# Kernel optimization log

Measured on AMD Instinct MI355X. Metric: run time of the kernel, lower is better.

## Reference

```python
import jax, jax.numpy as jnp
import numpy as np

EMBED_DIM = 1024
NUM_HEADS = 16
HEAD_DIM = EMBED_DIM // NUM_HEADS


def setup_inputs() -> dict:
    key = jax.random.key(0)
    k1, k2, k3, k4 = jax.random.split(key, 4)
    x = jax.random.normal(k1, (2, 2048, EMBED_DIM), dtype=jnp.float32)
    # nn.Linear weights: stored as [out, in]; we keep that convention.
    s = 1.0 / np.sqrt(EMBED_DIM)
    w_qkv = jax.random.uniform(k2, (3 * EMBED_DIM, EMBED_DIM), jnp.float32, -s, s)
    w_proj = jax.random.uniform(k3, (EMBED_DIM, EMBED_DIM), jnp.float32, -s, s)
    b_proj = jax.random.uniform(k4, (EMBED_DIM,), jnp.float32, -s, s)
    return {"x": x, "w_qkv": w_qkv, "w_proj": w_proj, "b_proj": b_proj}


def reference(x, w_qkv, w_proj, b_proj):
    B, N, C = x.shape
    H, D = NUM_HEADS, HEAD_DIM
    scale = D ** -0.5
    # qkv: [B, N, 3C] -> [3, B, H, N, D]
    qkv = jnp.einsum('bnc,oc->bno', x, w_qkv)
    qkv = qkv.reshape(B, N, 3, H, D).transpose(2, 0, 3, 1, 4)
    q, k, v = qkv[0] * scale, qkv[1], qkv[2]
    attn = jax.nn.softmax(jnp.einsum('bhnd,bhmd->bhnm', q, k), axis=-1)
    out = jnp.einsum('bhnm,bhmd->bhnd', attn, v)
    out = out.transpose(0, 2, 1, 3).reshape(B, N, C)
    return jnp.einsum('bnc,oc->bno', out, w_proj) + b_proj
```

## Files before the change

kernel.cpp:

```cpp
#include <hip/hip_runtime.h>


constexpr int B_ = 2, N_ = 2048, C_ = 1024, H_ = 16, D_ = 64;
constexpr int M_ = B_ * N_;
constexpr int O3 = 3 * C_;
constexpr int KVB = 64;
constexpr int NTILES = N_ / KVB;

typedef short bf16x8 __attribute__((ext_vector_type(8)));
typedef _Float16 half8 __attribute__((ext_vector_type(8)));
typedef _Float16 half4v __attribute__((ext_vector_type(4)));
typedef float f32x4  __attribute__((ext_vector_type(4)));

__device__ __forceinline__ unsigned short f2bf(float f) {
    unsigned int u = __float_as_uint(f);
    unsigned int r = (u + 0x7FFFu + ((u >> 16) & 1u)) >> 16;
    return (unsigned short)r;
}

__device__ __forceinline__ void async16(const void* g, void* l) {
    __builtin_amdgcn_global_load_lds(
        (const __attribute__((address_space(1))) unsigned int*)g,
        (__attribute__((address_space(3))) unsigned int*)l, 16, 0, 0);
}

constexpr size_t XN  = (size_t)M_ * C_;
constexpr size_t WQN = (size_t)O3 * C_;
constexpr size_t WPN = (size_t)C_ * C_;

__global__ __launch_bounds__(256)
void convert_f16(const float* __restrict__ x, const float* __restrict__ wq,
                 const float* __restrict__ wp, _Float16* __restrict__ dst)
{
    size_t i = ((size_t)blockIdx.x * 256 + threadIdx.x) * 8;
    const float* src;
    size_t off;
    if (i < XN)            { src = x;  off = i; }
    else if (i < XN + WQN) { src = wq; off = i - XN; }
    else                   { src = wp; off = i - XN - WQN; }
    float4 a = *(const float4*)(src + off);
    float4 b = *(const float4*)(src + off + 4);
    half8 h;
    h[0] = (_Float16)a.x; h[1] = (_Float16)a.y; h[2] = (_Float16)a.z; h[3] = (_Float16)a.w;
    h[4] = (_Float16)b.x; h[5] = (_Float16)b.y; h[6] = (_Float16)b.z; h[7] = (_Float16)b.w;
    *(half8*)(dst + i) = h;
}

template<int MODE>
__global__ __launch_bounds__(256)
void gemm128(const _Float16* __restrict__ Ag, const _Float16* __restrict__ Bg,
             unsigned short* __restrict__ Qd, unsigned short* __restrict__ Kd,
             unsigned short* __restrict__ Vt,
             const float* __restrict__ bias, float* __restrict__ Out)
{
    __shared__ __align__(16) unsigned char Ab[2][16384];
    __shared__ __align__(16) unsigned char Bb[2][16384];

    const int t    = threadIdx.x;
    const int lane = t & 63;
    const int w    = t >> 6;
    const int g    = lane >> 4;
    const int c    = lane & 15;
    const int wm   = w >> 1, wn = w & 1;
    const int bm   = blockIdx.y * 128;
    const int bn   = blockIdx.x * 128;
    constexpr int K = C_;

    f32x4 acc[4][4];
    f32x4 zero = {0.f, 0.f, 0.f, 0.f};
    #pragma unroll
    for (int mi = 0; mi < 4; ++mi)
        #pragma unroll
        for (int ni = 0; ni < 4; ++ni) acc[mi][ni] = zero;

    auto stage = [&](int buf, int k0) {
        #pragma unroll
        for (int i = 0; i < 4; ++i) {
            int id  = t + 256 * i;
            int row = id >> 3;
            int p   = id & 7;
            int gs  = p ^ (row & 7);
            async16(Ag + (size_t)(bm + row) * K + k0 + 8 * gs, &Ab[buf][id * 16]);
            async16(Bg + (size_t)(bn + row) * K + k0 + 8 * gs, &Bb[buf][id * 16]);
        }
    };

    stage(0, 0);
    __syncthreads();
    int cur = 0;

    for (int k0 = 0; k0 < K; k0 += 64) {
        if (k0 + 64 < K) stage(cur ^ 1, k0 + 64);

        const unsigned char* Abase = Ab[cur];
        const unsigned char* Bbase = Bb[cur];
        #pragma unroll
        for (int s = 0; s < 2; ++s) {
            half8 af[4], bf[4];
            #pragma unroll
            for (int mi = 0; mi < 4; ++mi) {
                int row = wm * 64 + mi * 16 + c;
                af[mi] = *(const half8*)(Abase + (row * 8 + ((s * 4 + g) ^ (row & 7))) * 16);
            }
            #pragma unroll
            for (int ni = 0; ni < 4; ++ni) {
                int row = wn * 64 + ni * 16 + c;
                bf[ni] = *(const half8*)(Bbase + (row * 8 + ((s * 4 + g) ^ (row & 7))) * 16);
            }
            #pragma unroll
            for (int mi = 0; mi < 4; ++mi)
                #pragma unroll
                for (int ni = 0; ni < 4; ++ni)
                    acc[mi][ni] = __builtin_amdgcn_mfma_f32_16x16x32_f16(af[mi], bf[ni], acc[mi][ni], 0, 0, 0);
        }

        __syncthreads();
        cur ^= 1;
    }

    if constexpr (MODE == 0) {
        constexpr float QSCALE = 0.125f * 1.4426950408889634f;
        const int o0 = bn + wn * 64;
        const int which = o0 >> 10;
        const int h  = (o0 & 1023) >> 6;
        const int m0 = bm + wm * 64;
        const int b  = m0 >> 11;
        const int n0 = m0 & 2047;
        const size_t bh = (size_t)b * H_ + h;
        if (which == 0) {
            unsigned short* base = Qd + (bh * N_) * D_;
            #pragma unroll
            for (int mi = 0; mi < 4; ++mi)
                #pragma unroll
                for (int ni = 0; ni < 4; ++ni)
                    #pragma unroll
                    for (int r = 0; r < 4; ++r)
                        base[(size_t)(n0 + mi * 16 + 4 * g + r) * D_ + ni * 16 + c] =
                            f2bf(acc[mi][ni][r] * QSCALE);
        } else if (which == 1) {
            unsigned short* base = Kd + (bh * N_) * D_;
            #pragma unroll
            for (int mi = 0; mi < 4; ++mi)
                #pragma unroll
                for (int ni = 0; ni < 4; ++ni)
                    #pragma unroll
                    for (int r = 0; r < 4; ++r)
                        base[(size_t)(n0 + mi * 16 + 4 * g + r) * D_ + ni * 16 + c] =
                            f2bf(acc[mi][ni][r]);
        } else {
            unsigned short* base = Vt + (bh * D_) * (size_t)N_;
            #pragma unroll
            for (int mi = 0; mi < 4; ++mi)
                #pragma unroll
                for (int ni = 0; ni < 4; ++ni) {
                    ushort4 v;
                    v.x = f2bf(acc[mi][ni][0]);
                    v.y = f2bf(acc[mi][ni][1]);
                    v.z = f2bf(acc[mi][ni][2]);
                    v.w = f2bf(acc[mi][ni][3]);
                    *(ushort4*)&base[(size_t)(ni * 16 + c) * N_ + n0 + mi * 16 + 4 * g] = v;
                }
        }
    } else {
        const int m0 = bm + wm * 64;
        const int o0 = bn + wn * 64;
        #pragma unroll
        for (int ni = 0; ni < 4; ++ni) {
            float bb = bias[o0 + ni * 16 + c];
            #pragma unroll
            for (int mi = 0; mi < 4; ++mi)
                #pragma unroll
                for (int r = 0; r < 4; ++r)
                    Out[(size_t)(m0 + mi * 16 + 4 * g + r) * C_ + o0 + ni * 16 + c] =
                        acc[mi][ni][r] + bb;
        }
    }
}

__global__ __launch_bounds__(512)
void attn_mfma(const unsigned short* __restrict__ Qd, const unsigned short* __restrict__ Kd,
               const unsigned short* __restrict__ Vt, _Float16* __restrict__ AO)
{
    __shared__ __align__(16) unsigned char KsB[2][64 * 128];
    __shared__ __align__(16) unsigned char VtB[2][64 * 128];
    __shared__ __align__(16) unsigned char Pb[8][16 * 128];

    const int t    = threadIdx.x;
    const int lane = t & 63;
    const int w    = t >> 6;
    const int g    = lane >> 4;
    const int c    = lane & 15;
    const int cx   = c & 7;

    int flat = blockIdx.x;
    int work = (flat & 7) * 64 + (flat >> 3);
    const int bh = work >> 4;
    const int qt = work & 15;
    const int b  = bh >> 4, h = bh & 15;
    const int q0 = qt * 128;

    const unsigned short* Kp = Kd + (size_t)bh * N_ * D_;
    const unsigned short* Vp = Vt + (size_t)bh * D_ * N_;

    const unsigned short* qp = Qd + ((size_t)bh * N_ + q0 + w * 16 + c) * D_;
    bf16x8 qf0 = *(const bf16x8*)(qp + 8 * g);
    bf16x8 qf1 = *(const bf16x8*)(qp + 32 + 8 * g);

    const int rk = t >> 3, pk = t & 7;
    const unsigned char* kSrc = (const unsigned char*)Kp + rk * 128 + ((pk ^ (rk & 7)) << 4);
    const unsigned char* vSrc = (const unsigned char*)Vp + (size_t)rk * N_ * 2 + ((pk ^ (rk & 7)) << 4);
    unsigned char* kDstA = KsB[0] + t * 16;
    unsigned char* kDstB = KsB[1] + t * 16;
    unsigned char* vDstA = VtB[0] + t * 16;
    unsigned char* vDstB = VtB[1] + t * 16;

    bf16x8 aone;
    {
        short onev = (c == 0) ? (short)0x3F80 : (short)0;
        #pragma unroll
        for (int e = 0; e < 8; ++e) aone[e] = onev;
    }

    float m_run = -1e30f;
    f32x4 oc[4];
    f32x4 lsum;
    f32x4 zero = {0.f, 0.f, 0.f, 0.f};
    #pragma unroll
    for (int dc = 0; dc < 4; ++dc) oc[dc] = zero;
    lsum = zero;

    async16(kSrc, kDstA);
    async16(vSrc, vDstA);
    __syncthreads();

    unsigned char* pw  = Pb[w] + c * 128;
    const unsigned char* prd = Pb[w] + c * 128;

    auto tile_body = [&](const unsigned char* kbase, const unsigned char* vb,
                         unsigned char* kDstN, unsigned char* vDstN, int ktNext) {
        if (ktNext < NTILES) {
            async16(kSrc + (size_t)ktNext * KVB * 128, kDstN);
            async16(vSrc + (size_t)ktNext * 128, vDstN);
        }

        f32x4 st[4];
        #pragma unroll
        for (int tt = 0; tt < 4; ++tt) st[tt] = zero;
        __builtin_amdgcn_s_setprio(1);
        #pragma unroll
        for (int s = 0; s < 2; ++s) {
            bf16x8 qf = s ? qf1 : qf0;
            #pragma unroll
            for (int tt = 0; tt < 4; ++tt) {
                bf16x8 a = *(const bf16x8*)(kbase + (tt * 16 + c) * 128 + (((4 * s + g) ^ cx) << 4));
                st[tt] = __builtin_amdgcn_mfma_f32_16x16x32_bf16(a, qf, st[tt], 0, 0, 0);
            }
        }
        __builtin_amdgcn_s_setprio(0);

        float t0 = fmaxf(fmaxf(st[0][0], st[0][1]), st[0][2]);
        float t1 = fmaxf(fmaxf(st[0][3], st[1][0]), st[1][1]);
        float t2 = fmaxf(fmaxf(st[1][2], st[1][3]), st[2][0]);
        float t3 = fmaxf(fmaxf(st[2][1], st[2][2]), st[2][3]);
        float t4 = fmaxf(fmaxf(st[3][0], st[3][1]), st[3][2]);
        float mx = fmaxf(fmaxf(fmaxf(t0, t1), fmaxf(t2, t3)), fmaxf(t4, st[3][3]));
        mx = fmaxf(mx, __shfl_xor(mx, 16));
        mx = fmaxf(mx, __shfl_xor(mx, 32));

        const bool defer = __all(mx <= m_run + 8.f);
        if (!defer) {
            const float nm = fmaxf(m_run, mx);
            const float corr = exp2f(m_run - nm);
            m_run = nm;
            #pragma unroll
            for (int dc = 0; dc < 4; ++dc) oc[dc] *= corr;
            lsum[0] *= corr;
        }
        const float nm = m_run;
        #pragma unroll
        for (int tt = 0; tt < 4; ++tt)
            #pragma unroll
            for (int r = 0; r < 4; ++r)
                st[tt][r] = exp2f(st[tt][r] - nm);

        #pragma unroll
        for (int tt = 0; tt < 4; ++tt) {
            unsigned int lo = __byte_perm(__float_as_uint(st[tt][0]), __float_as_uint(st[tt][1]), 0x7632);
            unsigned int hi = __byte_perm(__float_as_uint(st[tt][2]), __float_as_uint(st[tt][3]), 0x7632);
            int gran = 2 * tt + (g >> 1);
            unsigned int* dst = (unsigned int*)(pw + ((gran ^ cx) << 4) + 8 * (g & 1));
            dst[0] = lo;
            dst[1] = hi;
        }

        bf16x8 pb0 = *(const bf16x8*)(prd + ((g ^ cx) << 4));
        bf16x8 pb1 = *(const bf16x8*)(prd + (((4 + g) ^ cx) << 4));
        __builtin_amdgcn_s_setprio(1);
        #pragma unroll
        for (int dc = 0; dc < 4; ++dc) {
            const unsigned char* vrow = vb + (dc * 16 + c) * 128;
            bf16x8 a0 = *(const bf16x8*)(vrow + ((g ^ cx) << 4));
            bf16x8 a1 = *(const bf16x8*)(vrow + (((4 + g) ^ cx) << 4));
            oc[dc] = __builtin_amdgcn_mfma_f32_16x16x32_bf16(a0, pb0, oc[dc], 0, 0, 0);
            oc[dc] = __builtin_amdgcn_mfma_f32_16x16x32_bf16(a1, pb1, oc[dc], 0, 0, 0);
        }
        lsum = __builtin_amdgcn_mfma_f32_16x16x32_bf16(aone, pb0, lsum, 0, 0, 0);
        lsum = __builtin_amdgcn_mfma_f32_16x16x32_bf16(aone, pb1, lsum, 0, 0, 0);
        __builtin_amdgcn_s_setprio(0);

        __syncthreads();
    };

    #pragma unroll 1
    for (int kt = 0; kt < NTILES; kt += 2) {
        tile_body(KsB[0], VtB[0], kDstB, vDstB, kt + 1);
        tile_body(KsB[1], VtB[1], kDstA, vDstA, kt + 2);
    }

    float l = __shfl(lsum[0], c);
    float inv = 1.0f / l;
    int q = q0 + w * 16 + c;
    _Float16* aop = AO + ((size_t)b * N_ + q) * C_ + h * D_;
    #pragma unroll
    for (int dc = 0; dc < 4; ++dc) {
        half4v o;
        o[0] = (_Float16)(oc[dc][0] * inv);
        o[1] = (_Float16)(oc[dc][1] * inv);
        o[2] = (_Float16)(oc[dc][2] * inv);
        o[3] = (_Float16)(oc[dc][3] * inv);
        *(half4v*)(aop + dc * 16 + 4 * g) = o;
    }
}

extern "C" void kernel_launch(void* const* d_in, const int* in_sizes, int n_in,
                              void* d_out, int out_size, void* d_ws, size_t ws_size,
                              hipStream_t stream) {
    const float* x      = (const float*)d_in[0];
    const float* w_qkv  = (const float*)d_in[1];
    const float* w_proj = (const float*)d_in[2];
    const float* b_proj = (const float*)d_in[3];
    float* out = (float*)d_out;

    const size_t hd = (size_t)B_ * H_ * N_ * D_;
    unsigned short* Qd = (unsigned short*)d_ws;
    unsigned short* Kd = Qd + hd;
    unsigned short* Vt = Kd + hd;
    _Float16* AO  = (_Float16*)(Vt + hd);
    _Float16* x16 = AO + hd;
    _Float16* wq16 = x16 + XN;
    _Float16* wp16 = wq16 + WQN;

    convert_f16<<<4096, 256, 0, stream>>>(x, w_qkv, w_proj, x16);
    gemm128<0><<<dim3(O3 / 128, M_ / 128), 256, 0, stream>>>(
        x16, wq16, Qd, Kd, Vt, nullptr, nullptr);
    attn_mfma<<<dim3(512), 512, 0, stream>>>(Qd, Kd, Vt, AO);
    gemm128<1><<<dim3(C_ / 128, M_ / 128), 256, 0, stream>>>(
        AO, wp16, nullptr, nullptr, nullptr, b_proj, out);
}
```

Measured before the change: 134.6 us.

## Process two 16-row query sub-tiles per wave to reuse K/V LDS fragments

Each wave in the attention kernel now handles 32 query rows (two 16-row sub-tiles) instead of 16, so each block covers 256 queries and the grid halves to 256 blocks. Every K and V fragment read from LDS feeds two MFMAs, halving LDS traffic and global K/V loads per query. The cost is roughly doubled accumulator and score registers per lane, larger LDS buffers for P, and only 256 blocks on a 256-CU device, which may reduce occupancy and latency hiding.

```diff
diff --git a/kernel.cpp b/kernel.cpp
--- a/kernel.cpp
+++ b/kernel.cpp
@@ -177,13 +177,13 @@
     }
 }
 
-__global__ __launch_bounds__(512)
+__global__ __launch_bounds__(512, 2)
 void attn_mfma(const unsigned short* __restrict__ Qd, const unsigned short* __restrict__ Kd,
                const unsigned short* __restrict__ Vt, _Float16* __restrict__ AO)
 {
-    __shared__ __align__(16) unsigned char KsB[2][64 * 128];
-    __shared__ __align__(16) unsigned char VtB[2][64 * 128];
-    __shared__ __align__(16) unsigned char Pb[8][16 * 128];
+    __shared__ __align__(16) unsigned char KsB[2][8192];
+    __shared__ __align__(16) unsigned char VtB[2][8192];
+    __shared__ __align__(16) unsigned char Pb[8][4096];
 
     const int t    = threadIdx.x;
     const int lane = t & 63;
@@ -193,18 +193,22 @@
     const int cx   = c & 7;
 
     int flat = blockIdx.x;
-    int work = (flat & 7) * 64 + (flat >> 3);
-    const int bh = work >> 4;
-    const int qt = work & 15;
+    int work = (flat & 7) * 32 + (flat >> 3);
+    const int bh = work >> 3;
+    const int qt = work & 7;
     const int b  = bh >> 4, h = bh & 15;
-    const int q0 = qt * 128;
+    const int q0 = qt * 256;
 
     const unsigned short* Kp = Kd + (size_t)bh * N_ * D_;
     const unsigned short* Vp = Vt + (size_t)bh * D_ * N_;
 
-    const unsigned short* qp = Qd + ((size_t)bh * N_ + q0 + w * 16 + c) * D_;
-    bf16x8 qf0 = *(const bf16x8*)(qp + 8 * g);
-    bf16x8 qf1 = *(const bf16x8*)(qp + 32 + 8 * g);
+    const unsigned short* qp = Qd + ((size_t)bh * N_ + q0 + w * 32 + c) * D_;
+    bf16x8 qf[2][2];
+    #pragma unroll
+    for (int qs = 0; qs < 2; ++qs)
+        #pragma unroll
+        for (int s = 0; s < 2; ++s)
+            qf[qs][s] = *(const bf16x8*)(qp + qs * 16 * D_ + s * 32 + 8 * g);
 
     const int rk = t >> 3, pk = t & 7;
     const unsigned char* kSrc = (const unsigned char*)Kp + rk * 128 + ((pk ^ (rk & 7)) << 4);
@@ -221,20 +225,20 @@
         for (int e = 0; e < 8; ++e) aone[e] = onev;
     }
 
-    float m_run = -1e30f;
-    f32x4 oc[4];
-    f32x4 lsum;
+    float m_run[2] = {-1e30f, -1e30f};
+    f32x4 oc[2][4];
+    f32x4 lsum[2];
     f32x4 zero = {0.f, 0.f, 0.f, 0.f};
     #pragma unroll
-    for (int dc = 0; dc < 4; ++dc) oc[dc] = zero;
-    lsum = zero;
+    for (int qs = 0; qs < 2; ++qs) {
+        lsum[qs] = zero;
+        #pragma unroll
+        for (int dc = 0; dc < 4; ++dc) oc[qs][dc] = zero;
+    }
 
     async16(kSrc, kDstA);
     async16(vSrc, vDstA);
     __syncthreads();
-
-    unsigned char* pw  = Pb[w] + c * 128;
-    const unsigned char* prd = Pb[w] + c * 128;
 
     auto tile_body = [&](const unsigned char* kbase, const unsigned char* vb,
                          unsigned char* kDstN, unsigned char* vDstN, int ktNext) {
@@ -243,69 +247,86 @@
             async16(vSrc + (size_t)ktNext * 128, vDstN);
         }
 
-        f32x4 st[4];
-        #pragma unroll
-        for (int tt = 0; tt < 4; ++tt) st[tt] = zero;
+        f32x4 st[2][4];
+        #pragma unroll
+        for (int qs = 0; qs < 2; ++qs)
+            #pragma unroll
+            for (int tt = 0; tt < 4; ++tt) st[qs][tt] = zero;
         __builtin_amdgcn_s_setprio(1);
         #pragma unroll
         for (int s = 0; s < 2; ++s) {
-            bf16x8 qf = s ? qf1 : qf0;
             #pragma unroll
             for (int tt = 0; tt < 4; ++tt) {
                 bf16x8 a = *(const bf16x8*)(kbase + (tt * 16 + c) * 128 + (((4 * s + g) ^ cx) << 4));
-                st[tt] = __builtin_amdgcn_mfma_f32_16x16x32_bf16(a, qf, st[tt], 0, 0, 0);
+                st[0][tt] = __builtin_amdgcn_mfma_f32_16x16x32_bf16(a, qf[0][s], st[0][tt], 0, 0, 0);
+                st[1][tt] = __builtin_amdgcn_mfma_f32_16x16x32_bf16(a, qf[1][s], st[1][tt], 0, 0, 0);
             }
         }
         __builtin_amdgcn_s_setprio(0);
 
-        float t0 = fmaxf(fmaxf(st[0][0], st[0][1]), st[0][2]);
-        float t1 = fmaxf(fmaxf(st[0][3], st[1][0]), st[1][1]);
-        float t2 = fmaxf(fmaxf(st[1][2], st[1][3]), st[2][0]);
-        float t3 = fmaxf(fmaxf(st[2][1], st[2][2]), st[2][3]);
-        float t4 = fmaxf(fmaxf(st[3][0], st[3][1]), st[3][2]);
-        float mx = fmaxf(fmaxf(fmaxf(t0, t1), fmaxf(t2, t3)), fmaxf(t4, st[3][3]));
-        mx = fmaxf(mx, __shfl_xor(mx, 16));
-        mx = fmaxf(mx, __shfl_xor(mx, 32));
-
-        const bool defer = __all(mx <= m_run + 8.f);
+        float mx[2];
+        #pragma unroll
+        for (int qs = 0; qs < 2; ++qs) {
+            float t0 = fmaxf(fmaxf(st[qs][0][0], st[qs][0][1]), st[qs][0][2]);
+            float t1 = fmaxf(fmaxf(st[qs][0][3], st[qs][1][0]), st[qs][1][1]);
+            float t2 = fmaxf(fmaxf(st[qs][1][2], st[qs][1][3]), st[qs][2][0]);
+            float t3 = fmaxf(fmaxf(st[qs][2][1], st[qs][2][2]), st[qs][2][3]);
+            float t4 = fmaxf(fmaxf(st[qs][3][0], st[qs][3][1]), st[qs][3][2]);
+            float m  = fmaxf(fmaxf(fmaxf(t0, t1), fmaxf(t2, t3)), fmaxf(t4, st[qs][3][3]));
+            m = fmaxf(m, __shfl_xor(m, 16));
+            m = fmaxf(m, __shfl_xor(m, 32));
+            mx[qs] = m;
+        }
+
+        const bool defer = __all(fmaxf(mx[0] - m_run[0], mx[1] - m_run[1]) <= 8.f);
         if (!defer) {
-            const float nm = fmaxf(m_run, mx);
-            const float corr = exp2f(m_run - nm);
-            m_run = nm;
-            #pragma unroll
-            for (int dc = 0; dc < 4; ++dc) oc[dc] *= corr;
-            lsum[0] *= corr;
-        }
-        const float nm = m_run;
-        #pragma unroll
-        for (int tt = 0; tt < 4; ++tt)
-            #pragma unroll
-            for (int r = 0; r < 4; ++r)
-                st[tt][r] = exp2f(st[tt][r] - nm);
-
-        #pragma unroll
-        for (int tt = 0; tt < 4; ++tt) {
-            unsigned int lo = __byte_perm(__float_as_uint(st[tt][0]), __float_as_uint(st[tt][1]), 0x7632);
-            unsigned int hi = __byte_perm(__float_as_uint(st[tt][2]), __float_as_uint(st[tt][3]), 0x7632);
-            int gran = 2 * tt + (g >> 1);
-            unsigned int* dst = (unsigned int*)(pw + ((gran ^ cx) << 4) + 8 * (g & 1));
-            dst[0] = lo;
-            dst[1] = hi;
-        }
-
-        bf16x8 pb0 = *(const bf16x8*)(prd + ((g ^ cx) << 4));
-        bf16x8 pb1 = *(const bf16x8*)(prd + (((4 + g) ^ cx) << 4));
+            #pragma unroll
+            for (int qs = 0; qs < 2; ++qs) {
+                const float nm = fmaxf(m_run[qs], mx[qs]);
+                const float corr = exp2f(m_run[qs] - nm);
+                m_run[qs] = nm;
+                #pragma unroll
+                for (int dc = 0; dc < 4; ++dc) oc[qs][dc] *= corr;
+                lsum[qs][0] *= corr;
+            }
+        }
+        #pragma unroll
+        for (int qs = 0; qs < 2; ++qs)
+            #pragma unroll
+            for (int tt = 0; tt < 4; ++tt)
+                #pragma unroll
+                for (int r = 0; r < 4; ++r)
+                    st[qs][tt][r] = exp2f(st[qs][tt][r] - m_run[qs]);
+
+        #pragma unroll
+        for (int qs = 0; qs < 2; ++qs) {
+            unsigned char* pwq = Pb[w] + qs * 2048 + c * 128;
+            #pragma unroll
+            for (int tt = 0; tt < 4; ++tt) {
+                unsigned int lo = __byte_perm(__float_as_uint(st[qs][tt][0]), __float_as_uint(st[qs][tt][1]), 0x7632);
+                unsigned int hi = __byte_perm(__float_as_uint(st[qs][tt][2]), __float_as_uint(st[qs][tt][3]), 0x7632);
+                int gran = 2 * tt + (g >> 1);
+                unsigned int* dst = (unsigned int*)(pwq + ((gran ^ cx) << 4) + 8 * (g & 1));
+                dst[0] = lo;
+                dst[1] = hi;
+            }
+        }
+
+        const unsigned char* prd = Pb[w] + c * 128;
         __builtin_amdgcn_s_setprio(1);
         #pragma unroll
-        for (int dc = 0; dc < 4; ++dc) {
-            const unsigned char* vrow = vb + (dc * 16 + c) * 128;
-            bf16x8 a0 = *(const bf16x8*)(vrow + ((g ^ cx) << 4));
-            bf16x8 a1 = *(const bf16x8*)(vrow + (((4 + g) ^ cx) << 4));
-            oc[dc] = __builtin_amdgcn_mfma_f32_16x16x32_bf16(a0, pb0, oc[dc], 0, 0, 0);
-            oc[dc] = __builtin_amdgcn_mfma_f32_16x16x32_bf16(a1, pb1, oc[dc], 0, 0, 0);
-        }
-        lsum = __builtin_amdgcn_mfma_f32_16x16x32_bf16(aone, pb0, lsum, 0, 0, 0);
-        lsum = __builtin_amdgcn_mfma_f32_16x16x32_bf16(aone, pb1, lsum, 0, 0, 0);
+        for (int s = 0; s < 2; ++s) {
+            bf16x8 pb0 = *(const bf16x8*)(prd + (((s * 4 + g) ^ cx) << 4));
+            bf16x8 pb1 = *(const bf16x8*)(prd + 2048 + (((s * 4 + g) ^ cx) << 4));
+            #pragma unroll
+            for (int dc = 0; dc < 4; ++dc) {
+                bf16x8 a = *(const bf16x8*)(vb + (dc * 16 + c) * 128 + (((s * 4 + g) ^ cx) << 4));
+                oc[0][dc] = __builtin_amdgcn_mfma_f32_16x16x32_bf16(a, pb0, oc[0][dc], 0, 0, 0);
+                oc[1][dc] = __builtin_amdgcn_mfma_f32_16x16x32_bf16(a, pb1, oc[1][dc], 0, 0, 0);
+            }
+            lsum[0] = __builtin_amdgcn_mfma_f32_16x16x32_bf16(aone, pb0, lsum[0], 0, 0, 0);
+            lsum[1] = __builtin_amdgcn_mfma_f32_16x16x32_bf16(aone, pb1, lsum[1], 0, 0, 0);
+        }
         __builtin_amdgcn_s_setprio(0);
 
         __syncthreads();
@@ -317,18 +338,21 @@
         tile_body(KsB[1], VtB[1], kDstA, vDstA, kt + 2);
     }
 
-    float l = __shfl(lsum[0], c);
-    float inv = 1.0f / l;
-    int q = q0 + w * 16 + c;
-    _Float16* aop = AO + ((size_t)b * N_ + q) * C_ + h * D_;
     #pragma unroll
-    for (int dc = 0; dc < 4; ++dc) {
-        half4v o;
-        o[0] = (_Float16)(oc[dc][0] * inv);
-        o[1] = (_Float16)(oc[dc][1] * inv);
-        o[2] = (_Float16)(oc[dc][2] * inv);
-        o[3] = (_Float16)(oc[dc][3] * inv);
-        *(half4v*)(aop + dc * 16 + 4 * g) = o;
+    for (int qs = 0; qs < 2; ++qs) {
+        float l = __shfl(lsum[qs][0], c);
+        float inv = 1.0f / l;
+        int q = q0 + w * 32 + qs * 16 + c;
+        _Float16* aop = AO + ((size_t)b * N_ + q) * C_ + h * D_;
+        #pragma unroll
+        for (int dc = 0; dc < 4; ++dc) {
+            half4v o;
+            o[0] = (_Float16)(oc[qs][dc][0] * inv);
+            o[1] = (_Float16)(oc[qs][dc][1] * inv);
+            o[2] = (_Float16)(oc[qs][dc][2] * inv);
+            o[3] = (_Float16)(oc[qs][dc][3] * inv);
+            *(half4v*)(aop + dc * 16 + 4 * g) = o;
+        }
     }
 }
 
@@ -353,7 +377,7 @@
     convert_f16<<<4096, 256, 0, stream>>>(x, w_qkv, w_proj, x16);
     gemm128<0><<<dim3(O3 / 128, M_ / 128), 256, 0, stream>>>(
         x16, wq16, Qd, Kd, Vt, nullptr, nullptr);
-    attn_mfma<<<dim3(512), 512, 0, stream>>>(Qd, Kd, Vt, AO);
+    attn_mfma<<<dim3(256), 512, 0, stream>>>(Qd, Kd, Vt, AO);
     gemm128<1><<<dim3(C_ / 128, M_ / 128), 256, 0, stream>>>(
         AO, wp16, nullptr, nullptr, nullptr, b_proj, out);
 }
```

Result: slower. 140.2 us (+4.1%).

## Switch attention to 32x32x16 MFMA with register-resident P via permlane32 swap

Applied to the files above, without the earlier changes.

The attention kernel now uses 32x32x16 bf16 MFMA instead of 16x16x32, with 4 waves of 256 threads each handling 32 query rows. The softmax probabilities stay in registers and are rearranged with v_permlane32_swap into the B operand layout, so the per-wave LDS staging buffer and its round trip go away. The row sum is computed with VALU adds plus a shuffle, replacing the extra ones-vector MFMAs. The goal is fewer LDS accesses and MFMA instructions per tile. The cost is more accumulator registers per wave and twice the async loads per thread.

```diff
diff --git a/kernel.cpp b/kernel.cpp
--- a/kernel.cpp
+++ b/kernel.cpp
@@ -11,6 +11,7 @@
 typedef _Float16 half8 __attribute__((ext_vector_type(8)));
 typedef _Float16 half4v __attribute__((ext_vector_type(4)));
 typedef float f32x4  __attribute__((ext_vector_type(4)));
+typedef float f32x16 __attribute__((ext_vector_type(16)));
 
 __device__ __forceinline__ unsigned short f2bf(float f) {
     unsigned int u = __float_as_uint(f);
@@ -177,94 +178,84 @@
     }
 }
 
-__global__ __launch_bounds__(512)
+__global__ __launch_bounds__(256, 2)
 void attn_mfma(const unsigned short* __restrict__ Qd, const unsigned short* __restrict__ Kd,
                const unsigned short* __restrict__ Vt, _Float16* __restrict__ AO)
 {
-    __shared__ __align__(16) unsigned char KsB[2][64 * 128];
-    __shared__ __align__(16) unsigned char VtB[2][64 * 128];
-    __shared__ __align__(16) unsigned char Pb[8][16 * 128];
+    __shared__ __align__(16) unsigned char KsB[2][8192];
+    __shared__ __align__(16) unsigned char VtB[2][8192];
 
     const int t    = threadIdx.x;
     const int lane = t & 63;
     const int w    = t >> 6;
-    const int g    = lane >> 4;
-    const int c    = lane & 15;
-    const int cx   = c & 7;
+    const int h    = lane >> 5;
+    const int q31  = lane & 31;
+    const int qsw  = q31 & 7;
 
     int flat = blockIdx.x;
     int work = (flat & 7) * 64 + (flat >> 3);
     const int bh = work >> 4;
     const int qt = work & 15;
-    const int b  = bh >> 4, h = bh & 15;
+    const int b  = bh >> 4, hh = bh & 15;
     const int q0 = qt * 128;
 
     const unsigned short* Kp = Kd + (size_t)bh * N_ * D_;
     const unsigned short* Vp = Vt + (size_t)bh * D_ * N_;
 
-    const unsigned short* qp = Qd + ((size_t)bh * N_ + q0 + w * 16 + c) * D_;
-    bf16x8 qf0 = *(const bf16x8*)(qp + 8 * g);
-    bf16x8 qf1 = *(const bf16x8*)(qp + 32 + 8 * g);
+    const unsigned short* qp = Qd + ((size_t)bh * N_ + q0 + w * 32 + q31) * D_;
+    bf16x8 qf[4];
+    #pragma unroll
+    for (int s = 0; s < 4; ++s)
+        qf[s] = *(const bf16x8*)(qp + 16 * s + 8 * h);
 
     const int rk = t >> 3, pk = t & 7;
     const unsigned char* kSrc = (const unsigned char*)Kp + rk * 128 + ((pk ^ (rk & 7)) << 4);
-    const unsigned char* vSrc = (const unsigned char*)Vp + (size_t)rk * N_ * 2 + ((pk ^ (rk & 7)) << 4);
+    const unsigned char* vSrc = (const unsigned char*)Vp + (size_t)rk * (N_ * 2) + ((pk ^ (rk & 7)) << 4);
     unsigned char* kDstA = KsB[0] + t * 16;
     unsigned char* kDstB = KsB[1] + t * 16;
     unsigned char* vDstA = VtB[0] + t * 16;
     unsigned char* vDstB = VtB[1] + t * 16;
 
-    bf16x8 aone;
-    {
-        short onev = (c == 0) ? (short)0x3F80 : (short)0;
-        #pragma unroll
-        for (int e = 0; e < 8; ++e) aone[e] = onev;
-    }
-
-    float m_run = -1e30f;
-    f32x4 oc[4];
-    f32x4 lsum;
-    f32x4 zero = {0.f, 0.f, 0.f, 0.f};
-    #pragma unroll
-    for (int dc = 0; dc < 4; ++dc) oc[dc] = zero;
-    lsum = zero;
-
-    async16(kSrc, kDstA);
-    async16(vSrc, vDstA);
+    float m_run = -1e30f, l_run = 0.f;
+    f32x16 oc0 = 0.f, oc1 = 0.f;
+
+    auto stage = [&](unsigned char* kD, unsigned char* vD, int kt) {
+        async16(kSrc + (size_t)kt * 8192, kD);
+        async16(kSrc + (size_t)kt * 8192 + 4096, kD + 4096);
+        async16(vSrc + (size_t)kt * 128, vD);
+        async16(vSrc + 32 * (size_t)(N_ * 2) + (size_t)kt * 128, vD + 4096);
+    };
+
+    stage(kDstA, vDstA, 0);
     __syncthreads();
 
-    unsigned char* pw  = Pb[w] + c * 128;
-    const unsigned char* prd = Pb[w] + c * 128;
-
-    auto tile_body = [&](const unsigned char* kbase, const unsigned char* vb,
+    auto tile_body = [&](const unsigned char* kbase, const unsigned char* vbase,
                          unsigned char* kDstN, unsigned char* vDstN, int ktNext) {
-        if (ktNext < NTILES) {
-            async16(kSrc + (size_t)ktNext * KVB * 128, kDstN);
-            async16(vSrc + (size_t)ktNext * 128, vDstN);
-        }
-
-        f32x4 st[4];
-        #pragma unroll
-        for (int tt = 0; tt < 4; ++tt) st[tt] = zero;
+        if (ktNext < NTILES) stage(kDstN, vDstN, ktNext);
+
+        f32x16 st0 = 0.f, st1 = 0.f;
+        const unsigned char* krow0 = kbase + q31 * 128;
+        const unsigned char* krow1 = kbase + (32 + q31) * 128;
         __builtin_amdgcn_s_setprio(1);
         #pragma unroll
-        for (int s = 0; s < 2; ++s) {
-            bf16x8 qf = s ? qf1 : qf0;
-            #pragma unroll
-            for (int tt = 0; tt < 4; ++tt) {
-                bf16x8 a = *(const bf16x8*)(kbase + (tt * 16 + c) * 128 + (((4 * s + g) ^ cx) << 4));
-                st[tt] = __builtin_amdgcn_mfma_f32_16x16x32_bf16(a, qf, st[tt], 0, 0, 0);
-            }
+        for (int s = 0; s < 4; ++s) {
+            int go = ((2 * s + h) ^ qsw) << 4;
+            bf16x8 a0 = *(const bf16x8*)(krow0 + go);
+            bf16x8 a1 = *(const bf16x8*)(krow1 + go);
+            st0 = __builtin_amdgcn_mfma_f32_32x32x16_bf16(a0, qf[s], st0, 0, 0, 0);
+            st1 = __builtin_amdgcn_mfma_f32_32x32x16_bf16(a1, qf[s], st1, 0, 0, 0);
         }
         __builtin_amdgcn_s_setprio(0);
 
-        float t0 = fmaxf(fmaxf(st[0][0], st[0][1]), st[0][2]);
-        float t1 = fmaxf(fmaxf(st[0][3], st[1][0]), st[1][1]);
-        float t2 = fmaxf(fmaxf(st[1][2], st[1][3]), st[2][0]);
-        float t3 = fmaxf(fmaxf(st[2][1], st[2][2]), st[2][3]);
-        float t4 = fmaxf(fmaxf(st[3][0], st[3][1]), st[3][2]);
-        float mx = fmaxf(fmaxf(fmaxf(t0, t1), fmaxf(t2, t3)), fmaxf(t4, st[3][3]));
-        mx = fmaxf(mx, __shfl_xor(mx, 16));
+        f32x16 mm;
+        #pragma unroll
+        for (int r = 0; r < 16; ++r) mm[r] = fmaxf(st0[r], st1[r]);
+        float a0 = fmaxf(fmaxf(mm[0], mm[1]), mm[2]);
+        float a1 = fmaxf(fmaxf(mm[3], mm[4]), mm[5]);
+        float a2 = fmaxf(fmaxf(mm[6], mm[7]), mm[8]);
+        float a3 = fmaxf(fmaxf(mm[9], mm[10]), mm[11]);
+        float a4 = fmaxf(fmaxf(mm[12], mm[13]), mm[14]);
+        float mx = fmaxf(fmaxf(fmaxf(a0, a1), fmaxf(a2, a3)), fmaxf(a4, mm[15]));
         mx = fmaxf(mx, __shfl_xor(mx, 32));
 
         const bool defer = __all(mx <= m_run + 8.f);
@@ -272,40 +263,65 @@
             const float nm = fmaxf(m_run, mx);
             const float corr = exp2f(m_run - nm);
             m_run = nm;
-            #pragma unroll
-            for (int dc = 0; dc < 4; ++dc) oc[dc] *= corr;
-            lsum[0] *= corr;
-        }
-        const float nm = m_run;
-        #pragma unroll
-        for (int tt = 0; tt < 4; ++tt)
-            #pragma unroll
-            for (int r = 0; r < 4; ++r)
-                st[tt][r] = exp2f(st[tt][r] - nm);
-
-        #pragma unroll
-        for (int tt = 0; tt < 4; ++tt) {
-            unsigned int lo = __byte_perm(__float_as_uint(st[tt][0]), __float_as_uint(st[tt][1]), 0x7632);
-            unsigned int hi = __byte_perm(__float_as_uint(st[tt][2]), __float_as_uint(st[tt][3]), 0x7632);
-            int gran = 2 * tt + (g >> 1);
-            unsigned int* dst = (unsigned int*)(pw + ((gran ^ cx) << 4) + 8 * (g & 1));
-            dst[0] = lo;
-            dst[1] = hi;
-        }
-
-        bf16x8 pb0 = *(const bf16x8*)(prd + ((g ^ cx) << 4));
-        bf16x8 pb1 = *(const bf16x8*)(prd + (((4 + g) ^ cx) << 4));
+            oc0 *= corr;
+            oc1 *= corr;
+            l_run *= corr;
+        }
+        #pragma unroll
+        for (int r = 0; r < 16; ++r) {
+            st0[r] = exp2f(st0[r] - m_run);
+            st1[r] = exp2f(st1[r] - m_run);
+        }
+
+        f32x16 sv = st0 + st1;
+        float ts = ((sv[0] + sv[1]) + (sv[2] + sv[3])) + ((sv[4] + sv[5]) + (sv[6] + sv[7]))
+                 + ((sv[8] + sv[9]) + (sv[10] + sv[11])) + ((sv[12] + sv[13]) + (sv[14] + sv[15]));
+        ts += __shfl_xor(ts, 32);
+        l_run += ts;
+
+        unsigned int pkd[2][4][2];
+        #pragma unroll
+        for (int m = 0; m < 4; ++m)
+            #pragma unroll
+            for (int j = 0; j < 2; ++j) {
+                pkd[0][m][j] = __byte_perm(__float_as_uint(st0[4*m + 2*j]),
+                                           __float_as_uint(st0[4*m + 2*j + 1]), 0x7632);
+                pkd[1][m][j] = __byte_perm(__float_as_uint(st1[4*m + 2*j]),
+                                           __float_as_uint(st1[4*m + 2*j + 1]), 0x7632);
+            }
+
+        #pragma unroll
+        for (int kb = 0; kb < 2; ++kb)
+            #pragma unroll
+            for (int u = 0; u < 2; ++u)
+                #pragma unroll
+                for (int j = 0; j < 2; ++j)
+                    asm("v_permlane32_swap_b32 %0, %1"
+                        : "+v"(pkd[kb][2*u][j]), "+v"(pkd[kb][2*u+1][j]));
+
+        bf16x8 pb[4];
+        #pragma unroll
+        for (int s = 0; s < 4; ++s) {
+            const int kb = s >> 1, u = s & 1;
+            union { unsigned int d[4]; bf16x8 v; } uu;
+            uu.d[0] = pkd[kb][2*u][0];
+            uu.d[1] = pkd[kb][2*u][1];
+            uu.d[2] = pkd[kb][2*u+1][0];
+            uu.d[3] = pkd[kb][2*u+1][1];
+            pb[s] = uu.v;
+        }
+
+        const unsigned char* vrow0 = vbase + q31 * 128;
+        const unsigned char* vrow1 = vbase + (32 + q31) * 128;
         __builtin_amdgcn_s_setprio(1);
         #pragma unroll
-        for (int dc = 0; dc < 4; ++dc) {
-            const unsigned char* vrow = vb + (dc * 16 + c) * 128;
-            bf16x8 a0 = *(const bf16x8*)(vrow + ((g ^ cx) << 4));
-            bf16x8 a1 = *(const bf16x8*)(vrow + (((4 + g) ^ cx) << 4));
-            oc[dc] = __builtin_amdgcn_mfma_f32_16x16x32_bf16(a0, pb0, oc[dc], 0, 0, 0);
-            oc[dc] = __builtin_amdgcn_mfma_f32_16x16x32_bf16(a1, pb1, oc[dc], 0, 0, 0);
-        }
-        lsum = __builtin_amdgcn_mfma_f32_16x16x32_bf16(aone, pb0, lsum, 0, 0, 0);
-        lsum = __builtin_amdgcn_mfma_f32_16x16x32_bf16(aone, pb1, lsum, 0, 0, 0);
+        for (int s = 0; s < 4; ++s) {
+            int go = ((2 * s + h) ^ qsw) << 4;
+            bf16x8 va0 = *(const bf16x8*)(vrow0 + go);
+            bf16x8 va1 = *(const bf16x8*)(vrow1 + go);
+            oc0 = __builtin_amdgcn_mfma_f32_32x32x16_bf16(va0, pb[s], oc0, 0, 0, 0);
+            oc1 = __builtin_amdgcn_mfma_f32_32x32x16_bf16(va1, pb[s], oc1, 0, 0, 0);
+        }
         __builtin_amdgcn_s_setprio(0);
 
         __syncthreads();
@@ -317,18 +333,19 @@
         tile_body(KsB[1], VtB[1], kDstA, vDstA, kt + 2);
     }
 
-    float l = __shfl(lsum[0], c);
-    float inv = 1.0f / l;
-    int q = q0 + w * 16 + c;
-    _Float16* aop = AO + ((size_t)b * N_ + q) * C_ + h * D_;
+    float inv = 1.0f / l_run;
+    const int q = q0 + w * 32 + q31;
+    _Float16* aop = AO + ((size_t)b * N_ + q) * C_ + hh * D_;
     #pragma unroll
-    for (int dc = 0; dc < 4; ++dc) {
-        half4v o;
-        o[0] = (_Float16)(oc[dc][0] * inv);
-        o[1] = (_Float16)(oc[dc][1] * inv);
-        o[2] = (_Float16)(oc[dc][2] * inv);
-        o[3] = (_Float16)(oc[dc][3] * inv);
-        *(half4v*)(aop + dc * 16 + 4 * g) = o;
+    for (int m = 0; m < 4; ++m) {
+        half4v o0, o1;
+        #pragma unroll
+        for (int i = 0; i < 4; ++i) {
+            o0[i] = (_Float16)(oc0[4*m + i] * inv);
+            o1[i] = (_Float16)(oc1[4*m + i] * inv);
+        }
+        *(half4v*)(aop + 8 * m + 4 * h) = o0;
+        *(half4v*)(aop + 32 + 8 * m + 4 * h) = o1;
     }
 }
 
@@ -353,7 +370,7 @@
     convert_f16<<<4096, 256, 0, stream>>>(x, w_qkv, w_proj, x16);
     gemm128<0><<<dim3(O3 / 128, M_ / 128), 256, 0, stream>>>(
         x16, wq16, Qd, Kd, Vt, nullptr, nullptr);
-    attn_mfma<<<dim3(512), 512, 0, stream>>>(Qd, Kd, Vt, AO);
+    attn_mfma<<<dim3(512), 256, 0, stream>>>(Qd, Kd, Vt, AO);
     gemm128<1><<<dim3(C_ / 128, M_ / 128), 256, 0, stream>>>(
         AO, wp16, nullptr, nullptr, nullptr, b_proj, out);
 }
```

Result: slower. 140.0 us (+4.0%).
